# Optimization experiments

Hardware: AMD Instinct MI355X
Metric: run time of the kernel (lower is better)

Reference implementation:

```python
import jax, jax.numpy as jnp
import numpy as np

N_WORDS = 8192   # total words in batch (flattened ragged loop)
CHAR_LEN = 16    # chars per word (padded/fixed instance)
WORD_VOCAB = 50000
CHAR_VOCAB = 128
WORD_DIM = 300
CHAR_DIM = 64
CHAR_HID = 128   # per-direction LSTM hidden
INPUT_DIM = 512
INFO_DIM = WORD_DIM + 2 * CHAR_HID  # 556


def setup_inputs() -> dict:
    key = jax.random.key(0)
    ks = jax.random.split(key, 16)
    s_ih = 1.0 / np.sqrt(CHAR_DIM)
    s_hh = 1.0 / np.sqrt(CHAR_HID)
    s_out = 1.0 / np.sqrt(INFO_DIM)
    return {
        "word_ids": jax.random.randint(ks[0], (N_WORDS,), 0, WORD_VOCAB),
        "char_ids": jax.random.randint(ks[1], (N_WORDS, CHAR_LEN), 0, CHAR_VOCAB),
        "word_table": jax.random.normal(ks[2], (WORD_VOCAB, WORD_DIM), jnp.float32),
        "char_table": jax.random.normal(ks[3], (CHAR_VOCAB, CHAR_DIM), jnp.float32),
        "Wih_f": jax.random.uniform(ks[4], (4 * CHAR_HID, CHAR_DIM), jnp.float32, -s_ih, s_ih),
        "Whh_f": jax.random.uniform(ks[5], (4 * CHAR_HID, CHAR_HID), jnp.float32, -s_hh, s_hh),
        "bih_f": jax.random.uniform(ks[6], (4 * CHAR_HID,), jnp.float32, -s_hh, s_hh),
        "bhh_f": jax.random.uniform(ks[7], (4 * CHAR_HID,), jnp.float32, -s_hh, s_hh),
        "Wih_b": jax.random.uniform(ks[8], (4 * CHAR_HID, CHAR_DIM), jnp.float32, -s_ih, s_ih),
        "Whh_b": jax.random.uniform(ks[9], (4 * CHAR_HID, CHAR_HID), jnp.float32, -s_hh, s_hh),
        "bih_b": jax.random.uniform(ks[10], (4 * CHAR_HID,), jnp.float32, -s_hh, s_hh),
        "bhh_b": jax.random.uniform(ks[11], (4 * CHAR_HID,), jnp.float32, -s_hh, s_hh),
        "W_out": jax.random.uniform(ks[12], (INPUT_DIM, INFO_DIM), jnp.float32, -s_out, s_out),
        "b_out": jax.random.uniform(ks[13], (INPUT_DIM,), jnp.float32, -s_out, s_out),
    }


def _lstm_dir(x, Wih, Whh, bih, bhh, reverse):
    # x: [L, N, D] -> outputs [L, N, H]; PyTorch gate order i,f,g,o; zero init state.
    L, N, _ = x.shape
    H = Whh.shape[1]
    b = bih + bhh

    def step(carry, xt):
        h, c = carry
        gates = xt @ Wih.T + h @ Whh.T + b  # [N, 4H]
        i, f, g, o = jnp.split(gates, 4, axis=-1)
        c = jax.nn.sigmoid(f) * c + jax.nn.sigmoid(i) * jnp.tanh(g)
        h = jax.nn.sigmoid(o) * jnp.tanh(c)
        return (h, c), h

    init = (jnp.zeros((N, H), x.dtype), jnp.zeros((N, H), x.dtype))
    _, hs = jax.lax.scan(step, init, x, reverse=reverse)
    return hs


def reference(word_ids, char_ids, word_table, char_table,
              Wih_f, Whh_f, bih_f, bhh_f,
              Wih_b, Whh_b, bih_b, bhh_b,
              W_out, b_out):
    w = word_table[word_ids]                     # [N, WORD_DIM]
    ce = char_table[char_ids]                    # [N, L, CHAR_DIM]
    x = jnp.transpose(ce, (1, 0, 2))             # [L, N, CHAR_DIM]
    hf = _lstm_dir(x, Wih_f, Whh_f, bih_f, bhh_f, reverse=False)  # [L, N, H]
    hb = _lstm_dir(x, Wih_b, Whh_b, bih_b, bhh_b, reverse=True)   # [L, N, H]
    # torch.sum over char positions of bidirectional outputs
    char_feat = jnp.sum(jnp.concatenate([hf, hb], axis=-1), axis=0)  # [N, 2H]
    feat = jnp.concatenate([w, char_feat], axis=-1)                  # [N, INFO_DIM]
    return jnp.tanh(feat @ W_out.T + b_out)                          # [N, INPUT_DIM]
```

## Files before the change

kernel.cpp:

```cpp
#include <hip/hip_runtime.h>
#include <hip/hip_bf16.h>

typedef __bf16 bf16x8 __attribute__((ext_vector_type(8)));
typedef float  f32x4  __attribute__((ext_vector_type(4)));
typedef int    i32x4  __attribute__((ext_vector_type(4)));

#define N_WORDS   8192
#define CHAR_LEN  16
#define WORD_DIM  300
#define CHAR_DIM  64
#define HID       128
#define G4        512
#define INFO      556
#define KPAD      576
#define OUTD      512
#define WBL       32
#define WB        16
#define L2E       1.4426950408889634f

__device__ __forceinline__ float sig_(float x) {
    return __builtin_amdgcn_rcpf(1.0f + __builtin_amdgcn_exp2f(-L2E * x));
}
__device__ __forceinline__ float tanh_(float x) {
    return 1.0f - 2.0f * __builtin_amdgcn_rcpf(1.0f + __builtin_amdgcn_exp2f((2.0f * L2E) * x));
}

__global__ void prep_kernel(const float* __restrict__ char_table,
                            const float* __restrict__ Wih_f, const float* __restrict__ bih_f,
                            const float* __restrict__ bhh_f,
                            const float* __restrict__ Wih_b, const float* __restrict__ bih_b,
                            const float* __restrict__ bhh_b,
                            const float* __restrict__ W_out,
                            const float* __restrict__ Whh_f, const float* __restrict__ Whh_b,
                            float* __restrict__ preT,
                            __bf16* __restrict__ Wpad, __bf16* __restrict__ WhhB) {
    __shared__ float x[CHAR_DIM];
    if (blockIdx.x < 256) {
        const int dir = blockIdx.x & 1;
        const int cid = blockIdx.x >> 1;
        const float* Wih = dir ? Wih_b : Wih_f;
        const float* b1  = dir ? bih_b : bih_f;
        const float* b2  = dir ? bhh_b : bhh_f;
        if (threadIdx.x < CHAR_DIM) x[threadIdx.x] = char_table[cid * CHAR_DIM + threadIdx.x];
        __syncthreads();
        for (int g = threadIdx.x; g < G4; g += 256) {
            const f32x4* w4 = (const f32x4*)(Wih + g * CHAR_DIM);
            const f32x4* x4 = (const f32x4*)x;
            float s = b1[g] + b2[g];
            #pragma unroll
            for (int d = 0; d < CHAR_DIM / 4; ++d) {
                f32x4 wv = w4[d], xv = x4[d];
                s += wv[0]*xv[0] + wv[1]*xv[1] + wv[2]*xv[2] + wv[3]*xv[3];
            }
            int tt = g >> 7, j = g & (HID - 1);
            preT[(dir * 128 + cid) * G4 + j * 4 + tt] = s;
        }
    } else {
        int idx = (blockIdx.x - 256) * 256 + threadIdx.x;
        if (idx < OUTD * KPAD) {
            int row = idx / KPAD, col = idx - row * KPAD;
            Wpad[idx] = (col < INFO) ? (__bf16)W_out[row * INFO + col] : (__bf16)0.0f;
        } else {
            int j = idx - OUTD * KPAD;
            if (j < 2 * G4 * HID) {
                const float* src = (j < G4 * HID) ? Whh_f : Whh_b;
                int k = (j < G4 * HID) ? j : j - G4 * HID;
                WhhB[j] = (__bf16)src[k];
            }
        }
    }
}

__global__ __launch_bounds__(512, 2) void lstm_kernel(
        const int*   __restrict__ char_ids,
        const float* __restrict__ preT,
        const __bf16* __restrict__ WhhB,
        __bf16* __restrict__ char_feat) {
    const int dir = blockIdx.y;
    const int wb  = blockIdx.x * WBL;
    const __bf16* Whh = WhhB + dir * G4 * HID;
    const float* preD = preT + dir * 128 * G4;

    const int tid  = threadIdx.x;
    const int wave = tid >> 6;
    const int lane = tid & 63;
    const int col  = lane & 15;
    const int quad = lane >> 4;
    const int jbase = wave * 16;

    __shared__ __bf16 h_lds[2][WBL][136];
    __shared__ int    cidT[CHAR_LEN][WBL];

    {
        int w = tid >> 4, t = tid & 15;
        cidT[t][w] = char_ids[(wb + w) * CHAR_LEN + t] * (G4 * 4);
    }
    for (int i = tid; i < 2 * WBL * 136; i += 512) ((__bf16*)h_lds)[i] = (__bf16)0.0f;

    bf16x8 Bfrag[4][4];
    #pragma unroll
    for (int tt = 0; tt < 4; ++tt) {
        int row = tt * HID + jbase + col;
        #pragma unroll
        for (int ks = 0; ks < 4; ++ks)
            Bfrag[tt][ks] = *(const bf16x8*)(Whh + row * HID + ks * 32 + quad * 8);
    }

    const char* base_lane = (const char*)(preD + (jbase + col) * 4);

    float c[2][4] = {}, sumh[2][4] = {};

    __syncthreads();

    f32x4 nx[2][4];
    {
        const int tc0 = dir ? (CHAR_LEN - 1) : 0;
        #pragma unroll
        for (int mt = 0; mt < 2; ++mt) {
            i32x4 off = *(const i32x4*)(&cidT[tc0][mt * 16 + quad * 4]);
            #pragma unroll
            for (int r = 0; r < 4; ++r)
                nx[mt][r] = *(const f32x4*)(base_lane + off[r]);
        }
    }

    for (int t = 0; t < CHAR_LEN; ++t) {
        const __bf16 (*hc)[136] = h_lds[t & 1];
        __bf16 (*hn)[136] = h_lds[(t + 1) & 1];

        f32x4 acc[2][4];
        #pragma unroll
        for (int mt = 0; mt < 2; ++mt)
            #pragma unroll
            for (int tt = 0; tt < 4; ++tt)
                acc[mt][tt] = (f32x4){nx[mt][0][tt], nx[mt][1][tt], nx[mt][2][tt], nx[mt][3][tt]};

        {
            bf16x8 A0 = *(const bf16x8*)(&hc[col][quad * 8]);
            bf16x8 A1 = *(const bf16x8*)(&hc[16 + col][quad * 8]);
            #pragma unroll
            for (int tt = 0; tt < 4; ++tt) {
                acc[0][tt] = __builtin_amdgcn_mfma_f32_16x16x32_bf16(A0, Bfrag[tt][0], acc[0][tt], 0, 0, 0);
                acc[1][tt] = __builtin_amdgcn_mfma_f32_16x16x32_bf16(A1, Bfrag[tt][0], acc[1][tt], 0, 0, 0);
            }
        }

        if (t + 1 < CHAR_LEN) {
            const int tc = dir ? (CHAR_LEN - 2 - t) : (t + 1);
            #pragma unroll
            for (int mt = 0; mt < 2; ++mt) {
                i32x4 off = *(const i32x4*)(&cidT[tc][mt * 16 + quad * 4]);
                #pragma unroll
                for (int r = 0; r < 4; ++r)
                    nx[mt][r] = *(const f32x4*)(base_lane + off[r]);
            }
        }

        #pragma unroll
        for (int ks = 1; ks < 4; ++ks) {
            bf16x8 A0 = *(const bf16x8*)(&hc[col][ks * 32 + quad * 8]);
            bf16x8 A1 = *(const bf16x8*)(&hc[16 + col][ks * 32 + quad * 8]);
            #pragma unroll
            for (int tt = 0; tt < 4; ++tt) {
                acc[0][tt] = __builtin_amdgcn_mfma_f32_16x16x32_bf16(A0, Bfrag[tt][ks], acc[0][tt], 0, 0, 0);
                acc[1][tt] = __builtin_amdgcn_mfma_f32_16x16x32_bf16(A1, Bfrag[tt][ks], acc[1][tt], 0, 0, 0);
            }
        }

        #pragma unroll
        for (int mt = 0; mt < 2; ++mt)
            #pragma unroll
            for (int r = 0; r < 4; ++r) {
                float iv = sig_(acc[mt][0][r]);
                float fv = sig_(acc[mt][1][r]);
                float gv = tanh_(acc[mt][2][r]);
                float ov = sig_(acc[mt][3][r]);
                float cv = fv * c[mt][r] + iv * gv;
                c[mt][r] = cv;
                float hv = ov * tanh_(cv);
                sumh[mt][r] += hv;
                hn[mt * 16 + quad * 4 + r][jbase + col] = (__bf16)hv;
            }
        __syncthreads();
    }

    #pragma unroll
    for (int mt = 0; mt < 2; ++mt)
        #pragma unroll
        for (int r = 0; r < 4; ++r)
            char_feat[(wb + mt * 16 + quad * 4 + r) * 256 + dir * HID + jbase + col]
                = (__bf16)sumh[mt][r];
}

__global__ __launch_bounds__(256, 4) void out_kernel(
        const int*   __restrict__ word_ids,
        const float* __restrict__ word_table,
        const __bf16* __restrict__ char_feat,
        const __bf16* __restrict__ Wpad,
        const float* __restrict__ b_out,
        float* __restrict__ out) {
    const int wb  = blockIdx.x * WB;
    const int tid = threadIdx.x;
    const int wave = tid >> 6, lane = tid & 63, col = lane & 15, quad = lane >> 4;

    __shared__ __bf16 feat[WB][584];
    __shared__ int wid[WB];
    if (tid < WB) wid[tid] = word_ids[wb + tid];
    __syncthreads();
    for (int idx = tid; idx < WB * 75; idx += 256) {
        int row = idx / 75, ch = idx - row * 75;
        f32x4 v = *(const f32x4*)(word_table + wid[row] * WORD_DIM + ch * 4);
        __bf16* d = &feat[row][ch * 4];
        d[0] = (__bf16)v[0]; d[1] = (__bf16)v[1]; d[2] = (__bf16)v[2]; d[3] = (__bf16)v[3];
    }
    for (int idx = tid; idx < WB * 32; idx += 256) {
        int row = idx / 32, ch = idx - row * 32;
        bf16x8 v = *(const bf16x8*)(char_feat + (wb + row) * 256 + ch * 8);
        __bf16* d = &feat[row][WORD_DIM + ch * 8];
        #pragma unroll
        for (int e = 0; e < 8; ++e) d[e] = v[e];
    }
    for (int idx = tid; idx < WB * 28; idx += 256) {
        int row = idx / 28, cc = idx - row * 28;
        feat[row][INFO + cc] = (__bf16)0.0f;
    }
    __syncthreads();

    f32x4 acc[8];
    #pragma unroll
    for (int nt = 0; nt < 8; ++nt) acc[nt] = (f32x4){0.f, 0.f, 0.f, 0.f};

    #pragma unroll 2
    for (int kb = 0; kb < KPAD / 32; ++kb) {
        bf16x8 A = *(const bf16x8*)(&feat[col][kb * 32 + quad * 8]);
        #pragma unroll
        for (int nt = 0; nt < 8; ++nt) {
            int n = wave * 128 + nt * 16 + col;
            bf16x8 B = *(const bf16x8*)(Wpad + n * KPAD + kb * 32 + quad * 8);
            acc[nt] = __builtin_amdgcn_mfma_f32_16x16x32_bf16(A, B, acc[nt], 0, 0, 0);
        }
    }

    #pragma unroll
    for (int nt = 0; nt < 8; ++nt) {
        int n = wave * 128 + nt * 16 + col;
        float bo = b_out[n];
        #pragma unroll
        for (int r = 0; r < 4; ++r) {
            int word = wb + quad * 4 + r;
            out[word * OUTD + n] = tanh_(acc[nt][r] + bo);
        }
    }
}

extern "C" void kernel_launch(void* const* d_in, const int* in_sizes, int n_in,
                              void* d_out, int out_size, void* d_ws, size_t ws_size,
                              hipStream_t stream) {
    const int*   word_ids   = (const int*)d_in[0];
    const int*   char_ids   = (const int*)d_in[1];
    const float* word_table = (const float*)d_in[2];
    const float* char_table = (const float*)d_in[3];
    const float* Wih_f = (const float*)d_in[4];
    const float* Whh_f = (const float*)d_in[5];
    const float* bih_f = (const float*)d_in[6];
    const float* bhh_f = (const float*)d_in[7];
    const float* Wih_b = (const float*)d_in[8];
    const float* Whh_b = (const float*)d_in[9];
    const float* bih_b = (const float*)d_in[10];
    const float* bhh_b = (const float*)d_in[11];
    const float* W_out = (const float*)d_in[12];
    const float* b_out = (const float*)d_in[13];

    char* ws = (char*)d_ws;
    float*  preT      = (float*)ws;
    __bf16* WhhB      = (__bf16*)(ws + 524288);
    __bf16* Wpad      = (__bf16*)(ws + 524288 + 262144);
    __bf16* char_feat = (__bf16*)(ws + 524288 + 262144 + 589824);

    prep_kernel<<<256 + (OUTD * KPAD + 2 * G4 * HID + 255) / 256, 256, 0, stream>>>(
        char_table, Wih_f, bih_f, bhh_f, Wih_b, bih_b, bhh_b,
        W_out, Whh_f, Whh_b, preT, Wpad, WhhB);
    lstm_kernel<<<dim3(N_WORDS / WBL, 2), 512, 0, stream>>>(char_ids, preT, WhhB, char_feat);
    out_kernel<<<N_WORDS / WB, 256, 0, stream>>>(word_ids, word_table, char_feat, Wpad, b_out,
                                                 (float*)d_out);
}
```

Before: 222.2 us.

## Retile output projection to 32-word blocks with 16 waves each computing 2x2 MFMA tiles

Moves the output GEMM kernel from 16-word blocks of 4 waves (each wave covering 128 output columns) to 32-word blocks of 16 waves (each covering 32 columns across two 16-row tiles). Every W_out fragment loaded from global memory now feeds two MFMAs, halving total weight traffic, and the number of blocks halves. In exchange each block is larger with more LDS, and per-wave instruction-level parallelism is lower (4 accumulators instead of 8), which could reduce latency hiding.

```diff
diff --git a/kernel.cpp b/kernel.cpp
--- a/kernel.cpp
+++ b/kernel.cpp
@@ -15,7 +15,7 @@
 #define KPAD      576
 #define OUTD      512
 #define WBL       32
-#define WB        16
+#define WBO       32
 #define L2E       1.4426950408889634f
 
 __device__ __forceinline__ float sig_(float x) {
@@ -192,64 +192,74 @@
                 = (__bf16)sumh[mt][r];
 }
 
-__global__ __launch_bounds__(256, 4) void out_kernel(
+__global__ __launch_bounds__(1024, 4) void out_kernel(
         const int*   __restrict__ word_ids,
         const float* __restrict__ word_table,
         const __bf16* __restrict__ char_feat,
         const __bf16* __restrict__ Wpad,
         const float* __restrict__ b_out,
         float* __restrict__ out) {
-    const int wb  = blockIdx.x * WB;
+    const int wb  = blockIdx.x * WBO;
     const int tid = threadIdx.x;
     const int wave = tid >> 6, lane = tid & 63, col = lane & 15, quad = lane >> 4;
-
-    __shared__ __bf16 feat[WB][584];
-    __shared__ int wid[WB];
-    if (tid < WB) wid[tid] = word_ids[wb + tid];
+    const int nbase = wave * 32;
+
+    __shared__ __bf16 feat[WBO][584];
+    __shared__ int wid[WBO];
+    if (tid < WBO) wid[tid] = word_ids[wb + tid];
     __syncthreads();
-    for (int idx = tid; idx < WB * 75; idx += 256) {
+    for (int idx = tid; idx < WBO * 75; idx += 1024) {
         int row = idx / 75, ch = idx - row * 75;
         f32x4 v = *(const f32x4*)(word_table + wid[row] * WORD_DIM + ch * 4);
         __bf16* d = &feat[row][ch * 4];
         d[0] = (__bf16)v[0]; d[1] = (__bf16)v[1]; d[2] = (__bf16)v[2]; d[3] = (__bf16)v[3];
     }
-    for (int idx = tid; idx < WB * 32; idx += 256) {
-        int row = idx / 32, ch = idx - row * 32;
+    {
+        int row = tid >> 5, ch = tid & 31;
         bf16x8 v = *(const bf16x8*)(char_feat + (wb + row) * 256 + ch * 8);
         __bf16* d = &feat[row][WORD_DIM + ch * 8];
         #pragma unroll
         for (int e = 0; e < 8; ++e) d[e] = v[e];
     }
-    for (int idx = tid; idx < WB * 28; idx += 256) {
-        int row = idx / 28, cc = idx - row * 28;
+    if (tid < WBO * 28) {
+        int row = tid / 28, cc = tid - row * 28;
         feat[row][INFO + cc] = (__bf16)0.0f;
     }
     __syncthreads();
 
-    f32x4 acc[8];
-    #pragma unroll
-    for (int nt = 0; nt < 8; ++nt) acc[nt] = (f32x4){0.f, 0.f, 0.f, 0.f};
+    f32x4 acc[2][2];
+    #pragma unroll
+    for (int mt = 0; mt < 2; ++mt)
+        #pragma unroll
+        for (int nt = 0; nt < 2; ++nt) acc[mt][nt] = (f32x4){0.f, 0.f, 0.f, 0.f};
+
+    const __bf16* Wp0 = Wpad + (nbase + col) * KPAD;
+    const __bf16* Wp1 = Wpad + (nbase + 16 + col) * KPAD;
 
     #pragma unroll 2
     for (int kb = 0; kb < KPAD / 32; ++kb) {
-        bf16x8 A = *(const bf16x8*)(&feat[col][kb * 32 + quad * 8]);
-        #pragma unroll
-        for (int nt = 0; nt < 8; ++nt) {
-            int n = wave * 128 + nt * 16 + col;
-            bf16x8 B = *(const bf16x8*)(Wpad + n * KPAD + kb * 32 + quad * 8);
-            acc[nt] = __builtin_amdgcn_mfma_f32_16x16x32_bf16(A, B, acc[nt], 0, 0, 0);
-        }
-    }
-
-    #pragma unroll
-    for (int nt = 0; nt < 8; ++nt) {
-        int n = wave * 128 + nt * 16 + col;
+        const int ko = kb * 32 + quad * 8;
+        bf16x8 B0 = *(const bf16x8*)(Wp0 + ko);
+        bf16x8 B1 = *(const bf16x8*)(Wp1 + ko);
+        bf16x8 A0 = *(const bf16x8*)(&feat[col][ko]);
+        bf16x8 A1 = *(const bf16x8*)(&feat[16 + col][ko]);
+        acc[0][0] = __builtin_amdgcn_mfma_f32_16x16x32_bf16(A0, B0, acc[0][0], 0, 0, 0);
+        acc[1][0] = __builtin_amdgcn_mfma_f32_16x16x32_bf16(A1, B0, acc[1][0], 0, 0, 0);
+        acc[0][1] = __builtin_amdgcn_mfma_f32_16x16x32_bf16(A0, B1, acc[0][1], 0, 0, 0);
+        acc[1][1] = __builtin_amdgcn_mfma_f32_16x16x32_bf16(A1, B1, acc[1][1], 0, 0, 0);
+    }
+
+    #pragma unroll
+    for (int nt = 0; nt < 2; ++nt) {
+        int n = nbase + nt * 16 + col;
         float bo = b_out[n];
         #pragma unroll
-        for (int r = 0; r < 4; ++r) {
-            int word = wb + quad * 4 + r;
-            out[word * OUTD + n] = tanh_(acc[nt][r] + bo);
-        }
+        for (int mt = 0; mt < 2; ++mt)
+            #pragma unroll
+            for (int r = 0; r < 4; ++r) {
+                int word = wb + mt * 16 + quad * 4 + r;
+                out[word * OUTD + n] = tanh_(acc[mt][nt][r] + bo);
+            }
     }
 }
 
@@ -281,6 +291,6 @@
         char_table, Wih_f, bih_f, bhh_f, Wih_b, bih_b, bhh_b,
         W_out, Whh_f, Whh_b, preT, Wpad, WhhB);
     lstm_kernel<<<dim3(N_WORDS / WBL, 2), 512, 0, stream>>>(char_ids, preT, WhhB, char_feat);
-    out_kernel<<<N_WORDS / WB, 256, 0, stream>>>(word_ids, word_table, char_feat, Wpad, b_out,
-                                                 (float*)d_out);
-}
+    out_kernel<<<N_WORDS / WBO, 1024, 0, stream>>>(word_ids, word_table, char_feat, Wpad, b_out,
+                                                   (float*)d_out);
+}
```

Result: faster. 204.6 us, median of 2 (-8.0%).
